# Optimization experiments

Measured on AMD Instinct MI355X. Metric: run time of the kernel, lower is better.

## Reference

```python
import jax, jax.numpy as jnp
import numpy as np
import math

B, S, D, H = 2, 2048, 512, 8
HD = D // H

def setup_inputs() -> dict:
    key = jax.random.key(0)
    ks = jax.random.split(key, 13)
    scale = 1.0 / math.sqrt(D)
    inp = {
        "q_in": jax.random.normal(ks[0], (B, S, D), jnp.float32),
        "k_in": jax.random.normal(ks[1], (B, S, D), jnp.float32),
        "v_in": jax.random.normal(ks[2], (B, S, D), jnp.float32),
        "mask": jax.random.randint(ks[3], (B, 1, S, S), 0, 2, jnp.int32),
        "W1": jax.random.uniform(ks[4], (D, D), jnp.float32, -scale, scale),
        "b1": jax.random.uniform(ks[5], (D,), jnp.float32, -scale, scale),
        "W2": jax.random.uniform(ks[6], (D, D), jnp.float32, -scale, scale),
        "b2": jax.random.uniform(ks[7], (D,), jnp.float32, -scale, scale),
        "W3": jax.random.uniform(ks[8], (D, D), jnp.float32, -scale, scale),
        "b3": jax.random.uniform(ks[9], (D,), jnp.float32, -scale, scale),
        "Wo": jax.random.uniform(ks[10], (D, D), jnp.float32, -scale, scale),
        "bo": jax.random.uniform(ks[11], (D,), jnp.float32, -scale, scale),
    }
    return inp

def reference(q_in, k_in, v_in, mask, W1, b1, W2, b2, W3, b3, Wo, bo):
    # Linear projections (torch Linear: y = x @ W.T + b)
    q = q_in @ W1.T + b1  # [B,S,D]
    k = k_in @ W2.T + b2
    v = v_in @ W3.T + b3
    # split heads -> [B,H,S,HD]
    def split(x):
        return x.reshape(B, S, H, HD).transpose(0, 2, 1, 3)
    q, k, v = split(q), split(k), split(v)
    scores = jnp.einsum("bhqd,bhkd->bhqk", q, k) / math.sqrt(HD)
    scores = jnp.where(mask == 0, jnp.float32(-1e9), scores)
    attn = jax.nn.softmax(scores, axis=-1)
    out = jnp.einsum("bhqk,bhkd->bhqd", attn, v)  # [B,H,S,HD]
    out = out.transpose(0, 2, 1, 3).reshape(B, S, D)
    return out @ Wo.T + bo
```

## Files before the change

### kernel.cpp

```cpp
#include <hip/hip_runtime.h>
#include <hip/hip_bf16.h>
#include <math.h>

constexpr int B_ = 2, S_ = 2048, D_ = 512, H_ = 8, HD_ = 64;
constexpr int M_ = B_ * S_;
constexpr int NT_ = S_ / 64;
constexpr int NSPLIT = 2;
constexpr int NT2 = NT_ / NSPLIT;
constexpr int ROWS = B_ * S_ * H_;
constexpr int NGROUPS = (B_ * S_ * NT_) / 4;

typedef short s16x8 __attribute__((ext_vector_type(8)));
typedef float f32x4 __attribute__((ext_vector_type(4)));
typedef unsigned short u16;
typedef unsigned long long u64;

#define SWZ(b) ((b) ^ ((((b) >> 7) & 7) << 4))

constexpr float SCL = 0.18033688f;

static __device__ __forceinline__ unsigned int cvt_pk2(float lo, float hi) {
  __hip_bfloat162 h = __float22bfloat162_rn(make_float2(lo, hi));
  return *(unsigned int*)&h;
}
static __device__ __forceinline__ u16 cvt1(float f) {
  __hip_bfloat16 h = __float2bfloat16(f);
  return *(u16*)&h;
}
static __device__ __forceinline__ uint4 pack8(float4 a, float4 b) {
  uint4 r;
  r.x = cvt_pk2(a.x, a.y); r.y = cvt_pk2(a.z, a.w);
  r.z = cvt_pk2(b.x, b.y); r.w = cvt_pk2(b.z, b.w);
  return r;
}
static __device__ __forceinline__ float4 sum_scale(float4 a, float4 b, float s) {
  return make_float4((a.x + b.x) * s, (a.y + b.y) * s,
                     (a.z + b.z) * s, (a.w + b.w) * s);
}

#define QKV_STEP(BUF, T)                                                      \
  {                                                                           \
    const bool more_ = ((T) < 7);                                             \
    if (more_) {                                                              \
      const int o4 = ((T) + 1) * 16;                                          \
      fx[0] = Xb[o4];  fx[1] = Xb[o4 + 1];  fx[2] = Xb[o4 + 2];  fx[3] = Xb[o4 + 3]; \
      fw0[0] = W0b[o4]; fw0[1] = W0b[o4 + 1]; fw0[2] = W0b[o4 + 2]; fw0[3] = W0b[o4 + 3]; \
      fw1[0] = W1b[o4]; fw1[1] = W1b[o4 + 1]; fw1[2] = W1b[o4 + 2]; fw1[3] = W1b[o4 + 3]; \
    }                                                                         \
    __builtin_amdgcn_s_setprio(1);                                            \
    _Pragma("unroll")                                                         \
    for (int kw = 0; kw < 2; ++kw) {                                          \
      s16x8 af0 = *(const s16x8*)(shb + SWZ((BUF)*24576 + (wm*32 + l15)*128 + kw*64 + lg*16)); \
      s16x8 af1 = *(const s16x8*)(shb + SWZ((BUF)*24576 + (wm*32 + 16 + l15)*128 + kw*64 + lg*16)); \
      s16x8 b00 = *(const s16x8*)(shb + SWZ((BUF)*24576 + 8192 + (wn*32 + l15)*128 + kw*64 + lg*16)); \
      s16x8 b01 = *(const s16x8*)(shb + SWZ((BUF)*24576 + 8192 + (wn*32 + 16 + l15)*128 + kw*64 + lg*16)); \
      s16x8 b10 = *(const s16x8*)(shb + SWZ((BUF)*24576 + 16384 + (wn*32 + l15)*128 + kw*64 + lg*16)); \
      s16x8 b11 = *(const s16x8*)(shb + SWZ((BUF)*24576 + 16384 + (wn*32 + 16 + l15)*128 + kw*64 + lg*16)); \
      acc[0][0][0] = __builtin_amdgcn_mfma_f32_16x16x32_bf16(af0, b00, acc[0][0][0], 0, 0, 0); \
      acc[0][0][1] = __builtin_amdgcn_mfma_f32_16x16x32_bf16(af0, b01, acc[0][0][1], 0, 0, 0); \
      acc[0][1][0] = __builtin_amdgcn_mfma_f32_16x16x32_bf16(af1, b00, acc[0][1][0], 0, 0, 0); \
      acc[0][1][1] = __builtin_amdgcn_mfma_f32_16x16x32_bf16(af1, b01, acc[0][1][1], 0, 0, 0); \
      acc[1][0][0] = __builtin_amdgcn_mfma_f32_16x16x32_bf16(af0, b10, acc[1][0][0], 0, 0, 0); \
      acc[1][0][1] = __builtin_amdgcn_mfma_f32_16x16x32_bf16(af0, b11, acc[1][0][1], 0, 0, 0); \
      acc[1][1][0] = __builtin_amdgcn_mfma_f32_16x16x32_bf16(af1, b10, acc[1][1][0], 0, 0, 0); \
      acc[1][1][1] = __builtin_amdgcn_mfma_f32_16x16x32_bf16(af1, b11, acc[1][1][1], 0, 0, 0); \
    }                                                                         \
    __builtin_amdgcn_s_setprio(0);                                            \
    if (more_) {                                                              \
      char* p_ = shb + ((BUF) ^ 1) * 24576;                                   \
      *(uint4*)(p_ + SWZ(awb)) = pack8(fx[0], fx[1]);                         \
      *(uint4*)(p_ + SWZ(awb + 16)) = pack8(fx[2], fx[3]);                    \
      *(uint4*)(p_ + SWZ(b0wb)) = pack8(fw0[0], fw0[1]);                      \
      *(uint4*)(p_ + SWZ(b0wb + 16)) = pack8(fw0[2], fw0[3]);                 \
      *(uint4*)(p_ + SWZ(b1wb)) = pack8(fw1[0], fw1[1]);                      \
      *(uint4*)(p_ + SWZ(b1wb + 16)) = pack8(fw1[2], fw1[3]);                 \
    }                                                                         \
    __syncthreads();                                                          \
  }

__global__ __launch_bounds__(256) void gemm_qkv(
    const float* __restrict__ Xq, const float* __restrict__ Wq,
    const float* __restrict__ bq, u16* __restrict__ Yq,
    const float* __restrict__ Xk, const float* __restrict__ Wk,
    const float* __restrict__ bk, u16* __restrict__ Yk,
    const float* __restrict__ Xv, const float* __restrict__ Wv,
    const float* __restrict__ bv, u16* __restrict__ Yv,
    const int* __restrict__ mask, u64* __restrict__ mbits)
{
  const float* X; const float* W; const float* bias; u16* Y;
  const int z = blockIdx.z;
  if (z == 0)      { X = Xq; W = Wq; bias = bq; Y = Yq; }
  else if (z == 1) { X = Xk; W = Wk; bias = bk; Y = Yk; }
  else             { X = Xv; W = Wv; bias = bv; Y = Yv; }

  __shared__ __align__(128) char SH[2][24576];
  char* shb = &SH[0][0];

  const int tid = threadIdx.x;
  const int lane = tid & 63, w = tid >> 6;
  const int l15 = lane & 15, lg = lane >> 4;
  const int wm = w >> 1, wn = w & 1;
  const int m0 = blockIdx.x * 64, n0 = blockIdx.y * 128;
  const int sr = tid >> 2, sc = (tid & 3) * 16;

  const float4* Xb  = (const float4*)&X[(size_t)(m0 + sr) * D_ + sc];
  const float4* W0b = (const float4*)&W[(size_t)(n0 + sr) * D_ + sc];
  const float4* W1b = (const float4*)&W[(size_t)(n0 + 64 + sr) * D_ + sc];
  const int awb  = sr * 128 + (tid & 3) * 32;
  const int b0wb = 8192 + awb;
  const int b1wb = 16384 + awb;

  float4 fx[4], fw0[4], fw1[4];
#pragma unroll
  for (int i = 0; i < 4; ++i) { fx[i] = Xb[i]; fw0[i] = W0b[i]; fw1[i] = W1b[i]; }

  const int bid = blockIdx.x + blockIdx.y * gridDim.x +
                  blockIdx.z * gridDim.x * gridDim.y;
  const int gw = bid * 4 + w;
  int4 mv[10];
#pragma unroll
  for (int i = 0; i < 10; ++i)
    mv[i] = *(const int4*)&mask[(size_t)(gw + i * 3072) * 256 + lane * 4];
  const bool has10 = (gw + 10 * 3072) < NGROUPS;
  int4 mv10 = make_int4(0, 0, 0, 0);
  if (has10)
    mv10 = *(const int4*)&mask[(size_t)(gw + 10 * 3072) * 256 + lane * 4];
  __builtin_amdgcn_sched_barrier(0);

  f32x4 acc[2][2][2];
#pragma unroll
  for (int nh = 0; nh < 2; ++nh)
#pragma unroll
    for (int i = 0; i < 2; ++i)
#pragma unroll
      for (int j = 0; j < 2; ++j) acc[nh][i][j] = (f32x4){0.f, 0.f, 0.f, 0.f};

  {
    char* p = shb;
    *(uint4*)(p + SWZ(awb)) = pack8(fx[0], fx[1]);
    *(uint4*)(p + SWZ(awb + 16)) = pack8(fx[2], fx[3]);
    *(uint4*)(p + SWZ(b0wb)) = pack8(fw0[0], fw0[1]);
    *(uint4*)(p + SWZ(b0wb + 16)) = pack8(fw0[2], fw0[3]);
    *(uint4*)(p + SWZ(b1wb)) = pack8(fw1[0], fw1[1]);
    *(uint4*)(p + SWZ(b1wb + 16)) = pack8(fw1[2], fw1[3]);
  }
  __syncthreads();

#pragma unroll 1
  for (int tt = 0; tt < 8; tt += 2) {
    QKV_STEP(0, tt)
    QKV_STEP(1, tt + 1)
  }

  const float oscale = (z == 0) ? SCL : 1.0f;

  if (z != 2) {
#pragma unroll
    for (int nh = 0; nh < 2; ++nh) {
      float bias_v[2];
      bias_v[0] = bias[n0 + nh * 64 + wn * 32 + l15];
      bias_v[1] = bias[n0 + nh * 64 + wn * 32 + 16 + l15];
#pragma unroll
      for (int am = 0; am < 2; ++am)
#pragma unroll
        for (int bn = 0; bn < 2; ++bn)
#pragma unroll
          for (int j = 0; j < 4; ++j) {
            const int row = m0 + wm * 32 + am * 16 + lg * 4 + j;
            const int col = n0 + nh * 64 + wn * 32 + bn * 16 + l15;
            Y[(size_t)row * D_ + col] = cvt1((acc[nh][am][bn][j] + bias_v[bn]) * oscale);
          }
    }
  } else {
    const int batch = m0 >> 11, sb = m0 & (S_ - 1);
#pragma unroll
    for (int nh = 0; nh < 2; ++nh) {
      const int hh = blockIdx.y * 2 + nh;
      float bias_v[2];
      bias_v[0] = bias[n0 + nh * 64 + wn * 32 + l15];
      bias_v[1] = bias[n0 + nh * 64 + wn * 32 + 16 + l15];
      __syncthreads();
#pragma unroll
      for (int am = 0; am < 2; ++am)
#pragma unroll
        for (int bn = 0; bn < 2; ++bn) {
          const int dd = wn * 32 + bn * 16 + l15;
          const int sl = wm * 32 + am * 16 + lg * 4;
          ushort4 pk;
          pk.x = cvt1(acc[nh][am][bn][0] + bias_v[bn]);
          pk.y = cvt1(acc[nh][am][bn][1] + bias_v[bn]);
          pk.z = cvt1(acc[nh][am][bn][2] + bias_v[bn]);
          pk.w = cvt1(acc[nh][am][bn][3] + bias_v[bn]);
          *(ushort4*)(shb + SWZ(dd * 128 + sl * 2)) = pk;
        }
      __syncthreads();
      const int cr = sr * 128 + (tid & 3) * 32;
      uint4 c0 = *(uint4*)(shb + SWZ(cr));
      uint4 c1 = *(uint4*)(shb + SWZ(cr + 16));
      u16* dst = &Y[(((size_t)batch * H_ + hh) * 64 + sr) * S_ + sb + sc];
      *(uint4*)dst = c0;
      *(uint4*)(dst + 8) = c1;
    }
  }

#pragma unroll
  for (int i = 0; i < 10; ++i) {
    const int g = gw + i * 3072;
    u64 b0 = __ballot(mv[i].x != 0);
    u64 b1 = __ballot(mv[i].y != 0);
    u64 b2 = __ballot(mv[i].z != 0);
    u64 b3 = __ballot(mv[i].w != 0);
    if (lane < 4) {
      const int q = lane;
      u64 r = ((b0 >> (16 * q)) & 0xFFFFULL)
            | (((b1 >> (16 * q)) & 0xFFFFULL) << 16)
            | (((b2 >> (16 * q)) & 0xFFFFULL) << 32)
            | (((b3 >> (16 * q)) & 0xFFFFULL) << 48);
      mbits[(size_t)g * 4 + q] = r;
    }
  }
  {
    u64 b0 = __ballot(mv10.x != 0);
    u64 b1 = __ballot(mv10.y != 0);
    u64 b2 = __ballot(mv10.z != 0);
    u64 b3 = __ballot(mv10.w != 0);
    if (has10 && lane < 4) {
      const int g = gw + 10 * 3072;
      const int q = lane;
      u64 r = ((b0 >> (16 * q)) & 0xFFFFULL)
            | (((b1 >> (16 * q)) & 0xFFFFULL) << 16)
            | (((b2 >> (16 * q)) & 0xFFFFULL) << 32)
            | (((b3 >> (16 * q)) & 0xFFFFULL) << 48);
      mbits[(size_t)g * 4 + q] = r;
    }
  }
}

#define OPROJ_STEP(BUF, T)                                                    \
  {                                                                           \
    const bool more_ = ((T) < 7);                                             \
    if (more_) {                                                              \
      const int t1 = (T) + 1;                                                 \
      const float4* q0 = (const float4*)(poR + t1 * 64);                      \
      const float4* q1 = (const float4*)(poR + 2097152 + t1 * 64);            \
      float4 s0 = q0[0], s1 = q0[1], s2 = q0[2], s3 = q0[3];                  \
      float4 u0 = q1[0], u1 = q1[1], u2 = q1[2], u3 = q1[3];                  \
      const float li = 1.0f / (plR[t1] + plR[ROWS + t1]);                     \
      ax[0] = pack8(sum_scale(s0, u0, li), sum_scale(s1, u1, li));            \
      ax[1] = pack8(sum_scale(s2, u2, li), sum_scale(s3, u3, li));            \
      const int o4 = t1 * 16;                                                 \
      fw[0] = Wb[o4]; fw[1] = Wb[o4 + 1]; fw[2] = Wb[o4 + 2]; fw[3] = Wb[o4 + 3]; \
    }                                                                         \
    __builtin_amdgcn_s_setprio(1);                                            \
    _Pragma("unroll")                                                         \
    for (int kw = 0; kw < 2; ++kw) {                                          \
      s16x8 af0 = *(const s16x8*)(shb + SWZ((BUF)*16384 + (wm*32 + l15)*128 + kw*64 + lg*16)); \
      s16x8 af1 = *(const s16x8*)(shb + SWZ((BUF)*16384 + (wm*32 + 16 + l15)*128 + kw*64 + lg*16)); \
      s16x8 bf0 = *(const s16x8*)(shb + SWZ((BUF)*16384 + 8192 + (wn*32 + l15)*128 + kw*64 + lg*16)); \
      s16x8 bf1 = *(const s16x8*)(shb + SWZ((BUF)*16384 + 8192 + (wn*32 + 16 + l15)*128 + kw*64 + lg*16)); \
      acc[0][0] = __builtin_amdgcn_mfma_f32_16x16x32_bf16(af0, bf0, acc[0][0], 0, 0, 0); \
      acc[0][1] = __builtin_amdgcn_mfma_f32_16x16x32_bf16(af0, bf1, acc[0][1], 0, 0, 0); \
      acc[1][0] = __builtin_amdgcn_mfma_f32_16x16x32_bf16(af1, bf0, acc[1][0], 0, 0, 0); \
      acc[1][1] = __builtin_amdgcn_mfma_f32_16x16x32_bf16(af1, bf1, acc[1][1], 0, 0, 0); \
    }                                                                         \
    __builtin_amdgcn_s_setprio(0);                                            \
    if (more_) {                                                              \
      char* p_ = shb + ((BUF) ^ 1) * 16384;                                   \
      *(uint4*)(p_ + SWZ(awb)) = ax[0];                                       \
      *(uint4*)(p_ + SWZ(awb + 16)) = ax[1];                                  \
      *(uint4*)(p_ + SWZ(bwb)) = pack8(fw[0], fw[1]);                         \
      *(uint4*)(p_ + SWZ(bwb + 16)) = pack8(fw[2], fw[3]);                    \
    }                                                                         \
    __syncthreads();                                                          \
  }

__global__ __launch_bounds__(256) void gemm_oproj(
    const float* __restrict__ po, const float* __restrict__ pl,
    const float* __restrict__ W, const float* __restrict__ bias,
    float* __restrict__ Y)
{
  __shared__ __align__(128) u16 SH[2][2][64][64];
  char* shb = (char*)SH;

  const int tid = threadIdx.x;
  const int lane = tid & 63, w = tid >> 6;
  const int l15 = lane & 15, lg = lane >> 4;
  const int wm = w >> 1, wn = w & 1;
  const int m0 = blockIdx.x * 64, n0 = blockIdx.y * 64;
  const int sr = tid >> 2, sc = (tid & 3) * 16;

  const float* poR = po + (size_t)(m0 + sr) * 512 + sc;
  const float* plR = pl + (size_t)(m0 + sr) * 8;
  const float4* Wb = (const float4*)&W[(size_t)(n0 + sr) * D_ + sc];
  const int awb = sr * 128 + (tid & 3) * 32;
  const int bwb = 8192 + sr * 128 + (tid & 3) * 32;

  f32x4 acc[2][2];
#pragma unroll
  for (int i = 0; i < 2; ++i)
#pragma unroll
    for (int j = 0; j < 2; ++j) acc[i][j] = (f32x4){0.f, 0.f, 0.f, 0.f};

  uint4 ax[2]; float4 fw[4];
  {
    const float4* q0 = (const float4*)(poR);
    const float4* q1 = (const float4*)(poR + 2097152);
    float4 s0 = q0[0], s1 = q0[1], s2 = q0[2], s3 = q0[3];
    float4 u0 = q1[0], u1 = q1[1], u2 = q1[2], u3 = q1[3];
    const float li = 1.0f / (plR[0] + plR[ROWS]);
    ax[0] = pack8(sum_scale(s0, u0, li), sum_scale(s1, u1, li));
    ax[1] = pack8(sum_scale(s2, u2, li), sum_scale(s3, u3, li));
#pragma unroll
    for (int i = 0; i < 4; ++i) fw[i] = Wb[i];
    char* p = shb;
    *(uint4*)(p + SWZ(awb)) = ax[0];
    *(uint4*)(p + SWZ(awb + 16)) = ax[1];
    *(uint4*)(p + SWZ(bwb)) = pack8(fw[0], fw[1]);
    *(uint4*)(p + SWZ(bwb + 16)) = pack8(fw[2], fw[3]);
  }
  __syncthreads();

#pragma unroll 1
  for (int tt = 0; tt < 8; tt += 2) {
    OPROJ_STEP(0, tt)
    OPROJ_STEP(1, tt + 1)
  }

  float bias_v[2];
  bias_v[0] = bias[n0 + wn * 32 + l15];
  bias_v[1] = bias[n0 + wn * 32 + 16 + l15];
#pragma unroll
  for (int am = 0; am < 2; ++am)
#pragma unroll
    for (int bn = 0; bn < 2; ++bn)
#pragma unroll
      for (int j = 0; j < 4; ++j) {
        const int row = m0 + wm * 32 + am * 16 + lg * 4 + j;
        const int col = n0 + wn * 32 + bn * 16 + l15;
        Y[(size_t)row * D_ + col] = acc[am][bn][j] + bias_v[bn];
      }
}

__global__ __launch_bounds__(512) void attn_mfma(
    const u16* __restrict__ qp, const u16* __restrict__ kp,
    const u16* __restrict__ vt, const u64* __restrict__ mbits,
    float* __restrict__ po, float* __restrict__ pl)
{
  const int fid = blockIdx.x + 16 * (blockIdx.y + 8 * blockIdx.z);
  const int d = (fid & 7) * 64 + (fid >> 3);
  const int bx = d & 15, by = (d >> 4) & 7, bz = d >> 7;

  const int b = bz >> 1, half = bz & 1;
  const int h = by;
  const int q0 = bx * 128;
  const int kt0 = half * (S_ / NSPLIT);
  const int tid = threadIdx.x;
  const int lane = tid & 63;
  const int w = tid >> 6;
  const int l15 = lane & 15, lg = lane >> 4;

  __shared__ __align__(128) u16 KV[2][2][64][64];
  __shared__ __align__(128) u16 Pl[8][16][64];
  char* kvb = (char*)KV;
  char* plb = (char*)Pl;

  const int qr = q0 + w * 16;

  const u16* qrow = qp + ((size_t)b * S_ + qr + l15) * D_ + h * HD_;
  const s16x8 qf0 = *(const s16x8*)(qrow + lg * 8);
  const s16x8 qf1 = *(const s16x8*)(qrow + 32 + lg * 8);

  s16x8 onesf;
#pragma unroll
  for (int i = 0; i < 8; ++i) onesf[i] = (short)0x3F80;

  f32x4 out[4];
#pragma unroll
  for (int dt = 0; dt < 4; ++dt) out[dt] = (f32x4){0.f, 0.f, 0.f, 0.f};
  float l_s = 0.f;

  const int sr8 = tid >> 3;
  const int sc8 = (tid & 7) * 8;
  const u16* kbase = kp + (size_t)b * S_ * D_ + h * HD_;
  const u16* vbase = vt + (((size_t)b * H_ + h) * 64 + sr8) * (size_t)S_ + kt0 + sc8;
  const u64* mrow = mbits + ((size_t)b * S_ + qr + l15) * NT_ + half * NT2;

  const int mX = (l15 & 7) << 4;
  const int rd_lo = ((l15 << 7) + lg * 16) ^ mX;
  const int rd_hi = rd_lo ^ 64;
  const int wr_k = ((sr8 << 7) + (tid & 7) * 16) ^ ((sr8 & 7) << 4);
  const int pq = w * 2048 + l15 * 128;
  const int pw0 = (pq + lg * 8) ^ mX;
  const int pa_lo = (pq + lg * 16) ^ mX;
  const int pa_hi = pa_lo ^ 64;

  uint4 rk0, rv0;
  {
    const u16* ksrc = kbase + (size_t)(kt0 + sr8) * D_ + sc8;
    rk0 = *(const uint4*)ksrc;
    rv0 = *(const uint4*)vbase;
    *(uint4*)(kvb + wr_k) = rk0;
    *(uint4*)(kvb + wr_k + 8192) = rv0;
  }
  u64 msk = mrow[0];
  __syncthreads();

#pragma unroll 1
  for (int t = 0; t < NT2; ++t) {
    const int cur = t & 1;
    const bool more = (t + 1 < NT2);
    u64 msk_n = 0;
    if (more) {
      const int kt = (t + 1) * 64;
      rk0 = *(const uint4*)(kbase + (size_t)(kt0 + kt + sr8) * D_ + sc8);
      rv0 = *(const uint4*)(vbase + kt);
      msk_n = mrow[t + 1];
    }

    const unsigned mlo = (unsigned)(msk >> lg);
    const unsigned mhi = (unsigned)(msk >> (lg + 32));

    char* rb_lo = kvb + (cur << 14) + rd_lo;
    char* rb_hi = kvb + (cur << 14) + rd_hi;

    f32x4 z[4];
    __builtin_amdgcn_s_setprio(1);
#pragma unroll
    for (int t4 = 0; t4 < 4; ++t4) {
      s16x8 kb0 = *(const s16x8*)(rb_lo + t4 * 2048);
      s16x8 kb1 = *(const s16x8*)(rb_hi + t4 * 2048);
      f32x4 zz = (f32x4){0.f, 0.f, 0.f, 0.f};
      zz = __builtin_amdgcn_mfma_f32_16x16x32_bf16(kb0, qf0, zz, 0, 0, 0);
      zz = __builtin_amdgcn_mfma_f32_16x16x32_bf16(kb1, qf1, zz, 0, 0, 0);
      z[t4] = zz;
    }
    __builtin_amdgcn_s_setprio(0);

    float x[4][4];
#pragma unroll
    for (int t4 = 0; t4 < 4; ++t4) {
#pragma unroll
      for (int r = 0; r < 4; ++r) {
        const unsigned bit = (r < 2) ? ((mlo >> (16 * r + 4 * t4)) & 1u)
                                     : ((mhi >> (16 * (r - 2) + 4 * t4)) & 1u);
        float xv = bit ? z[t4][r] : -1.0e9f;
        x[t4][r] = exp2f(xv);
      }
    }

#pragma unroll
    for (int t4 = 0; t4 < 4; ++t4) {
      uint2 pk;
      pk.x = cvt_pk2(x[t4][0], x[t4][1]);
      pk.y = cvt_pk2(x[t4][2], x[t4][3]);
      *(uint2*)(plb + (pw0 ^ (t4 * 32))) = pk;
    }

    s16x8 pa0 = *(const s16x8*)(plb + pa_lo);
    s16x8 pa1 = *(const s16x8*)(plb + pa_hi);

    __builtin_amdgcn_s_setprio(1);
    f32x4 zl = (f32x4){0.f, 0.f, 0.f, 0.f};
    zl = __builtin_amdgcn_mfma_f32_16x16x32_bf16(onesf, pa0, zl, 0, 0, 0);
    zl = __builtin_amdgcn_mfma_f32_16x16x32_bf16(onesf, pa1, zl, 0, 0, 0);
#pragma unroll
    for (int dt = 0; dt < 4; ++dt) {
      s16x8 va0 = *(const s16x8*)(rb_lo + 8192 + dt * 2048);
      s16x8 va1 = *(const s16x8*)(rb_hi + 8192 + dt * 2048);
      out[dt] = __builtin_amdgcn_mfma_f32_16x16x32_bf16(va0, pa0, out[dt], 0, 0, 0);
      out[dt] = __builtin_amdgcn_mfma_f32_16x16x32_bf16(va1, pa1, out[dt], 0, 0, 0);
    }
    __builtin_amdgcn_s_setprio(0);
    l_s += zl[0];

    if (more) {
      char* wb = kvb + ((cur ^ 1) << 14) + wr_k;
      *(uint4*)(wb) = rk0;
      *(uint4*)(wb + 8192) = rv0;
      msk = msk_n;
    }
    __syncthreads();
  }

  const int rowi = ((b * S_ + qr + l15) * H_) + h;
  float* pobase = po + ((size_t)half * ROWS + rowi) * 64;
#pragma unroll
  for (int dt = 0; dt < 4; ++dt) {
    float4 o = make_float4(out[dt][0], out[dt][1], out[dt][2], out[dt][3]);
    *(float4*)&pobase[dt * 16 + lg * 4] = o;
  }
  if (lg == 0) pl[(size_t)half * ROWS + rowi] = l_s;
}

extern "C" void kernel_launch(void* const* d_in, const int* in_sizes, int n_in,
                              void* d_out, int out_size, void* d_ws,
                              size_t ws_size, hipStream_t stream)
{
  const float* q_in = (const float*)d_in[0];
  const float* k_in = (const float*)d_in[1];
  const float* v_in = (const float*)d_in[2];
  const int*   mask = (const int*)d_in[3];
  const float* W1 = (const float*)d_in[4];
  const float* b1 = (const float*)d_in[5];
  const float* W2 = (const float*)d_in[6];
  const float* b2 = (const float*)d_in[7];
  const float* W3 = (const float*)d_in[8];
  const float* b3 = (const float*)d_in[9];
  const float* Wo = (const float*)d_in[10];
  const float* bo = (const float*)d_in[11];
  float* out = (float*)d_out;

  char* ws = (char*)d_ws;
  u16* qp = (u16*)ws;
  u16* kp = (u16*)(ws + (4u << 20));
  u16* vtp = (u16*)(ws + (8u << 20));
  u64* mbits = (u64*)(ws + (12u << 20));
  float* pl = (float*)(ws + (13u << 20));
  float* po = (float*)(ws + (13u << 20) + (512u << 10));

  gemm_qkv<<<dim3(M_ / 64, D_ / 128, 3), dim3(256), 0, stream>>>(
      q_in, W1, b1, qp, k_in, W2, b2, kp, v_in, W3, b3, vtp, mask, mbits);
  attn_mfma<<<dim3(S_ / 128, H_, B_ * NSPLIT), dim3(512), 0, stream>>>(
      qp, kp, vtp, mbits, po, pl);
  gemm_oproj<<<dim3(M_ / 64, D_ / 64), dim3(256), 0, stream>>>(po, pl, Wo, bo, out);
}
```

Measured before the change: 90.34 us.

## Process two 64-key chunks per attention loop iteration to halve barriers

Each loop iteration of the attention kernel now stages 128 keys of K and V into shared memory and runs the score, softmax and PV steps twice, once per 64-key chunk. This halves the number of __syncthreads barriers and global-load rounds per block, and each thread issues two 16-byte loads per tensor per stage. In exchange shared memory for K/V doubles to 64 KB and register pressure rises from holding the extra prefetch registers, which may lower occupancy.

```diff
diff --git a/kernel.cpp b/kernel.cpp
--- a/kernel.cpp
+++ b/kernel.cpp
@@ -7,6 +7,7 @@
 constexpr int NT_ = S_ / 64;
 constexpr int NSPLIT = 2;
 constexpr int NT2 = NT_ / NSPLIT;
+constexpr int NTK = NT2 / 2;
 constexpr int ROWS = B_ * S_ * H_;
 constexpr int NGROUPS = (B_ * S_ * NT_) / 4;
 
@@ -341,6 +342,57 @@
       }
 }
 
+#define ATTN_CHUNK(C, MSKC)                                                   \
+  {                                                                           \
+    const unsigned mlo = (unsigned)((MSKC) >> lg);                            \
+    const unsigned mhi = (unsigned)((MSKC) >> (lg + 32));                     \
+    f32x4 z[4];                                                               \
+    __builtin_amdgcn_s_setprio(1);                                            \
+    _Pragma("unroll")                                                         \
+    for (int t4 = 0; t4 < 4; ++t4) {                                          \
+      s16x8 kb0 = *(const s16x8*)(rb_lo + (C) * 8192 + t4 * 2048);            \
+      s16x8 kb1 = *(const s16x8*)(rb_hi + (C) * 8192 + t4 * 2048);            \
+      f32x4 zz = (f32x4){0.f, 0.f, 0.f, 0.f};                                 \
+      zz = __builtin_amdgcn_mfma_f32_16x16x32_bf16(kb0, qf0, zz, 0, 0, 0);    \
+      zz = __builtin_amdgcn_mfma_f32_16x16x32_bf16(kb1, qf1, zz, 0, 0, 0);    \
+      z[t4] = zz;                                                             \
+    }                                                                         \
+    __builtin_amdgcn_s_setprio(0);                                            \
+    float x[4][4];                                                            \
+    _Pragma("unroll")                                                         \
+    for (int t4 = 0; t4 < 4; ++t4) {                                          \
+      _Pragma("unroll")                                                       \
+      for (int r = 0; r < 4; ++r) {                                           \
+        const unsigned bit = (r < 2) ? ((mlo >> (16 * r + 4 * t4)) & 1u)      \
+                                     : ((mhi >> (16 * (r - 2) + 4 * t4)) & 1u); \
+        float xv = bit ? z[t4][r] : -1.0e9f;                                  \
+        x[t4][r] = exp2f(xv);                                                 \
+      }                                                                       \
+    }                                                                         \
+    _Pragma("unroll")                                                         \
+    for (int t4 = 0; t4 < 4; ++t4) {                                          \
+      uint2 pk;                                                               \
+      pk.x = cvt_pk2(x[t4][0], x[t4][1]);                                     \
+      pk.y = cvt_pk2(x[t4][2], x[t4][3]);                                     \
+      *(uint2*)(plb + (pw0 ^ (t4 * 32))) = pk;                                \
+    }                                                                         \
+    s16x8 pa0 = *(const s16x8*)(plb + pa_lo);                                 \
+    s16x8 pa1 = *(const s16x8*)(plb + pa_hi);                                 \
+    __builtin_amdgcn_s_setprio(1);                                            \
+    f32x4 zl = (f32x4){0.f, 0.f, 0.f, 0.f};                                   \
+    zl = __builtin_amdgcn_mfma_f32_16x16x32_bf16(onesf, pa0, zl, 0, 0, 0);    \
+    zl = __builtin_amdgcn_mfma_f32_16x16x32_bf16(onesf, pa1, zl, 0, 0, 0);    \
+    _Pragma("unroll")                                                         \
+    for (int dt = 0; dt < 4; ++dt) {                                          \
+      s16x8 va0 = *(const s16x8*)(rb_lo + 16384 + (C) * 8192 + dt * 2048);    \
+      s16x8 va1 = *(const s16x8*)(rb_hi + 16384 + (C) * 8192 + dt * 2048);    \
+      out[dt] = __builtin_amdgcn_mfma_f32_16x16x32_bf16(va0, pa0, out[dt], 0, 0, 0); \
+      out[dt] = __builtin_amdgcn_mfma_f32_16x16x32_bf16(va1, pa1, out[dt], 0, 0, 0); \
+    }                                                                         \
+    __builtin_amdgcn_s_setprio(0);                                            \
+    l_s += zl[0];                                                             \
+  }
+
 __global__ __launch_bounds__(512) void attn_mfma(
     const u16* __restrict__ qp, const u16* __restrict__ kp,
     const u16* __restrict__ vt, const u64* __restrict__ mbits,
@@ -359,7 +411,7 @@
   const int w = tid >> 6;
   const int l15 = lane & 15, lg = lane >> 4;
 
-  __shared__ __align__(128) u16 KV[2][2][64][64];
+  __shared__ __align__(128) u16 KV[2][2][128][64];
   __shared__ __align__(128) u16 Pl[8][16][64];
   char* kvb = (char*)KV;
   char* plb = (char*)Pl;
@@ -379,105 +431,66 @@
   for (int dt = 0; dt < 4; ++dt) out[dt] = (f32x4){0.f, 0.f, 0.f, 0.f};
   float l_s = 0.f;
 
-  const int sr8 = tid >> 3;
-  const int sc8 = (tid & 7) * 8;
+  const int krow = tid >> 2;
+  const int kc = (tid & 3) * 16;
+  const int vrow = tid >> 3;
+  const int vsel = (tid >> 2) & 1;
   const u16* kbase = kp + (size_t)b * S_ * D_ + h * HD_;
-  const u16* vbase = vt + (((size_t)b * H_ + h) * 64 + sr8) * (size_t)S_ + kt0 + sc8;
+  const u16* vbase = vt + (((size_t)b * H_ + h) * 64 + vrow) * (size_t)S_
+                     + kt0 + vsel * 64 + kc;
   const u64* mrow = mbits + ((size_t)b * S_ + qr + l15) * NT_ + half * NT2;
 
   const int mX = (l15 & 7) << 4;
   const int rd_lo = ((l15 << 7) + lg * 16) ^ mX;
   const int rd_hi = rd_lo ^ 64;
-  const int wr_k = ((sr8 << 7) + (tid & 7) * 16) ^ ((sr8 & 7) << 4);
+  const int wr_k = ((krow << 7) + (tid & 3) * 32) ^ ((krow & 7) << 4);
+  const int wr_v = 16384 + vsel * 8192 +
+                   (((vrow << 7) + (tid & 3) * 32) ^ ((vrow & 7) << 4));
   const int pq = w * 2048 + l15 * 128;
   const int pw0 = (pq + lg * 8) ^ mX;
   const int pa_lo = (pq + lg * 16) ^ mX;
   const int pa_hi = pa_lo ^ 64;
 
-  uint4 rk0, rv0;
+  uint4 rk0, rk1, rv0, rv1;
   {
-    const u16* ksrc = kbase + (size_t)(kt0 + sr8) * D_ + sc8;
-    rk0 = *(const uint4*)ksrc;
-    rv0 = *(const uint4*)vbase;
+    const u16* ksrc = kbase + (size_t)(kt0 + krow) * D_ + kc;
+    rk0 = *(const uint4*)ksrc; rk1 = *(const uint4*)(ksrc + 8);
+    rv0 = *(const uint4*)vbase; rv1 = *(const uint4*)(vbase + 8);
     *(uint4*)(kvb + wr_k) = rk0;
-    *(uint4*)(kvb + wr_k + 8192) = rv0;
-  }
-  u64 msk = mrow[0];
+    *(uint4*)(kvb + (wr_k ^ 16)) = rk1;
+    *(uint4*)(kvb + wr_v) = rv0;
+    *(uint4*)(kvb + (wr_v ^ 16)) = rv1;
+  }
+  u64 msk0 = mrow[0], msk1 = mrow[1];
   __syncthreads();
 
 #pragma unroll 1
-  for (int t = 0; t < NT2; ++t) {
+  for (int t = 0; t < NTK; ++t) {
     const int cur = t & 1;
-    const bool more = (t + 1 < NT2);
-    u64 msk_n = 0;
+    const bool more = (t + 1 < NTK);
+    u64 mskn0 = 0, mskn1 = 0;
     if (more) {
-      const int kt = (t + 1) * 64;
-      rk0 = *(const uint4*)(kbase + (size_t)(kt0 + kt + sr8) * D_ + sc8);
-      rv0 = *(const uint4*)(vbase + kt);
-      msk_n = mrow[t + 1];
+      const int kt = (t + 1) * 128;
+      const u16* ksrc = kbase + (size_t)(kt0 + kt + krow) * D_ + kc;
+      rk0 = *(const uint4*)ksrc; rk1 = *(const uint4*)(ksrc + 8);
+      rv0 = *(const uint4*)(vbase + kt); rv1 = *(const uint4*)(vbase + kt + 8);
+      mskn0 = mrow[2 * t + 2];
+      mskn1 = mrow[2 * t + 3];
     }
 
-    const unsigned mlo = (unsigned)(msk >> lg);
-    const unsigned mhi = (unsigned)(msk >> (lg + 32));
-
-    char* rb_lo = kvb + (cur << 14) + rd_lo;
-    char* rb_hi = kvb + (cur << 14) + rd_hi;
-
-    f32x4 z[4];
-    __builtin_amdgcn_s_setprio(1);
-#pragma unroll
-    for (int t4 = 0; t4 < 4; ++t4) {
-      s16x8 kb0 = *(const s16x8*)(rb_lo + t4 * 2048);
-      s16x8 kb1 = *(const s16x8*)(rb_hi + t4 * 2048);
-      f32x4 zz = (f32x4){0.f, 0.f, 0.f, 0.f};
-      zz = __builtin_amdgcn_mfma_f32_16x16x32_bf16(kb0, qf0, zz, 0, 0, 0);
-      zz = __builtin_amdgcn_mfma_f32_16x16x32_bf16(kb1, qf1, zz, 0, 0, 0);
-      z[t4] = zz;
-    }
-    __builtin_amdgcn_s_setprio(0);
-
-    float x[4][4];
-#pragma unroll
-    for (int t4 = 0; t4 < 4; ++t4) {
-#pragma unroll
-      for (int r = 0; r < 4; ++r) {
-        const unsigned bit = (r < 2) ? ((mlo >> (16 * r + 4 * t4)) & 1u)
-                                     : ((mhi >> (16 * (r - 2) + 4 * t4)) & 1u);
-        float xv = bit ? z[t4][r] : -1.0e9f;
-        x[t4][r] = exp2f(xv);
-      }
-    }
-
-#pragma unroll
-    for (int t4 = 0; t4 < 4; ++t4) {
-      uint2 pk;
-      pk.x = cvt_pk2(x[t4][0], x[t4][1]);
-      pk.y = cvt_pk2(x[t4][2], x[t4][3]);
-      *(uint2*)(plb + (pw0 ^ (t4 * 32))) = pk;
-    }
-
-    s16x8 pa0 = *(const s16x8*)(plb + pa_lo);
-    s16x8 pa1 = *(const s16x8*)(plb + pa_hi);
-
-    __builtin_amdgcn_s_setprio(1);
-    f32x4 zl = (f32x4){0.f, 0.f, 0.f, 0.f};
-    zl = __builtin_amdgcn_mfma_f32_16x16x32_bf16(onesf, pa0, zl, 0, 0, 0);
-    zl = __builtin_amdgcn_mfma_f32_16x16x32_bf16(onesf, pa1, zl, 0, 0, 0);
-#pragma unroll
-    for (int dt = 0; dt < 4; ++dt) {
-      s16x8 va0 = *(const s16x8*)(rb_lo + 8192 + dt * 2048);
-      s16x8 va1 = *(const s16x8*)(rb_hi + 8192 + dt * 2048);
-      out[dt] = __builtin_amdgcn_mfma_f32_16x16x32_bf16(va0, pa0, out[dt], 0, 0, 0);
-      out[dt] = __builtin_amdgcn_mfma_f32_16x16x32_bf16(va1, pa1, out[dt], 0, 0, 0);
-    }
-    __builtin_amdgcn_s_setprio(0);
-    l_s += zl[0];
+    char* rb_lo = kvb + (cur << 15) + rd_lo;
+    char* rb_hi = kvb + (cur << 15) + rd_hi;
+
+    ATTN_CHUNK(0, msk0)
+    ATTN_CHUNK(1, msk1)
 
     if (more) {
-      char* wb = kvb + ((cur ^ 1) << 14) + wr_k;
-      *(uint4*)(wb) = rk0;
-      *(uint4*)(wb + 8192) = rv0;
-      msk = msk_n;
+      char* wb = kvb + ((cur ^ 1) << 15);
+      *(uint4*)(wb + wr_k) = rk0;
+      *(uint4*)(wb + (wr_k ^ 16)) = rk1;
+      *(uint4*)(wb + wr_v) = rv0;
+      *(uint4*)(wb + (wr_v ^ 16)) = rv1;
+      msk0 = mskn0; msk1 = mskn1;
     }
     __syncthreads();
   }
```

Measured after the change: 88.72 us. About the same (-1.8%).
